# Performance work log

Measured on AMD Instinct MI355X. Metric: run time of the kernel, lower is better.

## Reference

```python
import jax, jax.numpy as jnp
import numpy as np

N_HEADS = 16
D_MODEL = 1024
D_K = D_MODEL // N_HEADS
B, T = 2, 2048


def setup_inputs() -> dict:
    key = jax.random.key(0)
    ks = jax.random.split(key, 12)
    s = 1.0 / np.sqrt(D_MODEL)
    inp = {
        "q": jax.random.normal(ks[0], (B, T, D_MODEL), jnp.float32),
        "k": jax.random.normal(ks[1], (B, T, D_MODEL), jnp.float32),
        "v": jax.random.normal(ks[2], (B, T, D_MODEL), jnp.float32),
        # weights stored as [in, out] (torch Linear weight transposed)
        "Wq": jax.random.normal(ks[3], (D_MODEL, D_MODEL), jnp.float32) * s,
        "bq": jax.random.normal(ks[4], (D_MODEL,), jnp.float32) * s,
        "Wk": jax.random.normal(ks[5], (D_MODEL, D_MODEL), jnp.float32) * s,
        "bk": jax.random.normal(ks[6], (D_MODEL,), jnp.float32) * s,
        "Wv": jax.random.normal(ks[7], (D_MODEL, D_MODEL), jnp.float32) * s,
        "bv": jax.random.normal(ks[8], (D_MODEL,), jnp.float32) * s,
        "Wo": jax.random.normal(ks[9], (D_MODEL, D_MODEL), jnp.float32) * s,
        "bo": jax.random.normal(ks[10], (D_MODEL,), jnp.float32) * s,
        "alpha": jnp.ones((1, N_HEADS, 1, 1), jnp.float32) * 10.0,
    }
    return inp


def reference(q, k, v, Wq, bq, Wk, bk, Wv, bv, Wo, bo, alpha):
    Bsz, Tlen, _ = q.shape

    def proj(x, W, b):
        # [B,T,D] -> [B,H,T,d_k]
        y = x @ W + b
        return y.reshape(Bsz, Tlen, N_HEADS, D_K).transpose(0, 2, 1, 3)

    qh = proj(q, Wq, bq)
    kh = proj(k, Wk, bk)
    vh = proj(v, Wv, bv)

    scores = jnp.einsum("bhqd,bhkd->bhqk", qh, kh)  # [B,H,T,T]
    norm_q = jnp.linalg.norm(qh, axis=-1)  # [B,H,T]
    norm_k = jnp.linalg.norm(kh, axis=-1)  # [B,H,T]
    D_udps = (norm_q[..., :, None] + norm_k[..., None, :]) ** 2  # [B,H,T,T]
    D_safe = jnp.where(D_udps == 0.0, jnp.inf, D_udps)
    scores = alpha * 4.0 * scores / D_safe
    attn = jax.nn.softmax(scores, axis=-1)
    out = jnp.einsum("bhqk,bhkd->bhqd", attn, vh)
    out = out.transpose(0, 2, 1, 3).reshape(Bsz, Tlen, D_MODEL)
    return out @ Wo + bo
```

## Files before the change

kernel.cpp:

```cpp
#include <hip/hip_runtime.h>
#include <hip/hip_bf16.h>

#define N_HEADS 16
#define D_MODEL 1024
#define D_K     64
#define B_SZ    2
#define T_LEN   2048
#define M_ROWS  (B_SZ * T_LEN)

typedef __bf16 bf16;
typedef __bf16 bf16x4 __attribute__((ext_vector_type(4)));
typedef __bf16 bf16x8 __attribute__((ext_vector_type(8)));
typedef float  f32x4  __attribute__((ext_vector_type(4)));
typedef unsigned int u32;

__device__ __forceinline__ void gload16(const bf16* g, bf16* l) {
    __builtin_amdgcn_global_load_lds(
        (const __attribute__((address_space(1))) u32*)g,
        (__attribute__((address_space(3))) u32*)l, 16, 0, 0);
}

__global__ void wt_kernel(const float* __restrict__ W0, const float* __restrict__ W1,
                          const float* __restrict__ W2, const float* __restrict__ W3,
                          bf16* __restrict__ T0, bf16* __restrict__ T1,
                          bf16* __restrict__ T2, bf16* __restrict__ T3) {
    __shared__ float tile[32][33];
    const int z = blockIdx.z;
    const float* W = (z == 0) ? W0 : (z == 1) ? W1 : (z == 2) ? W2 : W3;
    bf16* Wt       = (z == 0) ? T0 : (z == 1) ? T1 : (z == 2) ? T2 : T3;
    const int tx = threadIdx.x, ty = threadIdx.y;
    const int x0 = blockIdx.x * 32, y0 = blockIdx.y * 32;
    for (int yy = ty; yy < 32; yy += 8)
        tile[yy][tx] = W[(size_t)(y0 + yy) * D_MODEL + x0 + tx];
    __syncthreads();
    for (int yy = ty; yy < 32; yy += 8)
        Wt[(size_t)(x0 + yy) * D_MODEL + y0 + tx] = (bf16)tile[tx][yy];
}

__global__ void conv3_kernel(const float* __restrict__ q, const float* __restrict__ k,
                             const float* __restrict__ v,
                             bf16* __restrict__ qb, bf16* __restrict__ kb,
                             bf16* __restrict__ vb) {
    const int z = blockIdx.y;
    const float* X = (z == 0) ? q : (z == 1) ? k : v;
    bf16* Y        = (z == 0) ? qb : (z == 1) ? kb : vb;
    const size_t i = ((size_t)blockIdx.x * 256 + threadIdx.x) * 8;
    const float4 v0 = *(const float4*)&X[i];
    const float4 v1 = *(const float4*)&X[i + 4];
    bf16x8 y;
    y[0]=(bf16)v0.x; y[1]=(bf16)v0.y; y[2]=(bf16)v0.z; y[3]=(bf16)v0.w;
    y[4]=(bf16)v1.x; y[5]=(bf16)v1.y; y[6]=(bf16)v1.z; y[7]=(bf16)v1.w;
    *(bf16x8*)&Y[i] = y;
}

__global__ __launch_bounds__(256, 3) void proj_kernel(
    const bf16* __restrict__ qb, const bf16* __restrict__ kb, const bf16* __restrict__ vb,
    const bf16* __restrict__ WtQ, const bf16* __restrict__ WtK, const bf16* __restrict__ WtV,
    const float* __restrict__ bqp, const float* __restrict__ bkp, const float* __restrict__ bvp,
    bf16* __restrict__ qh, bf16* __restrict__ kh, bf16* __restrict__ vt)
{
    __shared__ bf16 As[2][128 * 32];
    __shared__ bf16 Bs[2][128 * 32];

    const int hw      = blockIdx.x;
    const int logical = (hw & 7) * 96 + (hw >> 3);
    const int z       = logical >> 8;
    const int r       = logical & 255;
    const int m0      = (r >> 3) * 128;
    const int n0      = (r & 7) * 128;

    const bf16*  A    = (z == 0) ? qb  : (z == 1) ? kb  : vb;
    const bf16*  Bt   = (z == 0) ? WtQ : (z == 1) ? WtK : WtV;
    const float* bias = (z == 0) ? bqp : (z == 1) ? bkp : bvp;
    bf16* Out         = (z == 0) ? qh  : (z == 1) ? kh  : vt;

    const int tid = threadIdx.x, lane = tid & 63, w = tid >> 6;
    const int wm = w >> 1, wn = w & 1, g = lane >> 4, c = lane & 15;

    const int srow = w * 32 + (lane >> 2);
    const int scol = (lane & 3) * 8;
    const bf16* Ag = A  + (size_t)(m0 + srow) * D_MODEL + scol;
    const bf16* Bg = Bt + (size_t)(n0 + srow) * D_MODEL + scol;

    f32x4 acc[4][4] = {};

#define PSTAGE(buf, kk)                                                         \
    do {                                                                        \
        gload16(Ag + (kk),                  &As[buf][(w * 32) * 32]);           \
        gload16(Ag + 16 * D_MODEL + (kk),   &As[buf][(w * 32 + 16) * 32]);      \
        gload16(Bg + (kk),                  &Bs[buf][(w * 32) * 32]);           \
        gload16(Bg + 16 * D_MODEL + (kk),   &Bs[buf][(w * 32 + 16) * 32]);      \
    } while (0)

    PSTAGE(0, 0);
    __syncthreads();

    int cur = 0;
    for (int t = 0; t < 32; ++t) {
        if (t < 31) PSTAGE(cur ^ 1, (t + 1) * 32);

        bf16x8 a[4], b[4];
        #pragma unroll
        for (int i = 0; i < 4; i++) a[i] = *(const bf16x8*)&As[cur][(wm*64 + i*16 + c) * 32 + g*8];
        #pragma unroll
        for (int j = 0; j < 4; j++) b[j] = *(const bf16x8*)&Bs[cur][(wn*64 + j*16 + c) * 32 + g*8];

        __builtin_amdgcn_s_setprio(1);
        if (z != 2) {
            #pragma unroll
            for (int i = 0; i < 4; i++)
                #pragma unroll
                for (int j = 0; j < 4; j++)
                    acc[i][j] = __builtin_amdgcn_mfma_f32_16x16x32_bf16(a[i], b[j], acc[i][j], 0, 0, 0);
        } else {
            #pragma unroll
            for (int i = 0; i < 4; i++)
                #pragma unroll
                for (int j = 0; j < 4; j++)
                    acc[i][j] = __builtin_amdgcn_mfma_f32_16x16x32_bf16(b[j], a[i], acc[i][j], 0, 0, 0);
        }
        __builtin_amdgcn_s_setprio(0);
        __syncthreads();
        cur ^= 1;
    }
#undef PSTAGE

    #pragma unroll
    for (int i = 0; i < 4; i++)
        #pragma unroll
        for (int j = 0; j < 4; j++)
            #pragma unroll
            for (int r4 = 0; r4 < 4; r4++) {
                if (z != 2) {
                    const int mrow = m0 + wm*64 + i*16 + g*4 + r4;
                    const int ncol = n0 + wn*64 + j*16 + c;
                    const float y = acc[i][j][r4] + bias[ncol];
                    const int b_ = mrow >> 11, t_ = mrow & (T_LEN - 1);
                    const int h_ = ncol >> 6,  d_ = ncol & (D_K - 1);
                    Out[(((size_t)(b_*N_HEADS + h_))*T_LEN + t_)*D_K + d_] = (bf16)y;
                } else {
                    const int nrow = n0 + wn*64 + j*16 + g*4 + r4;
                    const int mcol = m0 + wm*64 + i*16 + c;
                    const float y = acc[i][j][r4] + bias[nrow];
                    const int b_ = mcol >> 11, t_ = mcol & (T_LEN - 1);
                    const int h_ = nrow >> 6,  d_ = nrow & (D_K - 1);
                    Out[(((size_t)(b_*N_HEADS + h_))*D_K + d_)*T_LEN + t_] = (bf16)y;
                }
            }
}

__global__ void norm_kernel(const bf16* __restrict__ qh, const bf16* __restrict__ kh,
                            float* __restrict__ nq, float* __restrict__ nk, int nrows) {
    const bf16* X = blockIdx.y ? kh : qh;
    float* O      = blockIdx.y ? nk : nq;
    const int row  = blockIdx.x * 4 + (threadIdx.x >> 6);
    const int lane = threadIdx.x & 63;
    if (row >= nrows) return;
    float v = (float)X[(size_t)row * D_K + lane];
    float s = v * v;
    #pragma unroll
    for (int m = 1; m < 64; m <<= 1) s += __shfl_xor(s, m, 64);
    if (lane == 0) O[row] = sqrtf(s);
}

#define KVB 64

__global__ __launch_bounds__(512, 4) void attn_kernel(
    const bf16* __restrict__ qh, const bf16* __restrict__ kh, const bf16* __restrict__ vt,
    const float* __restrict__ nq, const float* __restrict__ nk,
    const float* __restrict__ alpha, bf16* __restrict__ ao)
{
    __shared__ bf16 Ks[2][KVB * D_K];
    __shared__ bf16 Vs[2][KVB * D_K];
    __shared__ bf16 plds[8][16][72];

    const int bid     = blockIdx.x;
    const int logical = (bid & 7) * 64 + (bid >> 3);
    const int bh      = logical >> 4;
    const int q0b     = (logical & 15) * 128;

    const int tid  = threadIdx.x;
    const int w    = tid >> 6;
    const int lane = tid & 63;
    const int g    = lane >> 4, c = lane & 15;
    const int myq  = q0b + w * 16 + c;
    const int sw   = (c & 7) << 4;

    const int srow = tid >> 3;
    const int sgb  = (((tid & 7) ^ (srow & 7)) << 4);

    const bf16* Q  = qh + (size_t)bh * T_LEN * D_K;
    const bf16* K  = kh + (size_t)bh * T_LEN * D_K;
    const bf16* V  = vt + (size_t)bh * D_K * T_LEN;
    const float* NK = nk + (size_t)bh * T_LEN;

    const float al   = alpha[bh & (N_HEADS - 1)];
    const float a4   = al * 4.0f * 1.44269504f;
    const float negM = -(al * 1.44269504f) - 1e-4f;

    const bf16x8 bq0 = *(const bf16x8*)&Q[(size_t)myq * D_K + g*8];
    const bf16x8 bq1 = *(const bf16x8*)&Q[(size_t)myq * D_K + 32 + g*8];
    const float nq_own = nq[(size_t)bh * T_LEN + myq];

    bf16x8 ones;
    #pragma unroll
    for (int e = 0; e < 8; e++) ones[e] = (bf16)1.0f;

    f32x4 o[4] = {};
    f32x4 o4  = {};

    gload16((const bf16*)((const char*)&K[(size_t)srow * D_K] + sgb), &Ks[0][w * 512]);
    gload16((const bf16*)((const char*)&V[(size_t)srow * T_LEN] + sgb), &Vs[0][w * 512]);
    __syncthreads();

    const int NT = T_LEN / KVB;
    int cur = 0;
    for (int t = 0; t < NT; ++t) {
        const int k0 = t * KVB;
        if (t + 1 < NT) {
            const int kn = k0 + KVB;
            gload16((const bf16*)((const char*)&K[(size_t)(kn + srow) * D_K] + sgb), &Ks[cur^1][w * 512]);
            gload16((const bf16*)((const char*)&V[(size_t)srow * T_LEN + kn] + sgb), &Vs[cur^1][w * 512]);
        }

        f32x4 S[4];
        __builtin_amdgcn_s_setprio(1);
        #pragma unroll
        for (int cb = 0; cb < 4; cb++) {
            const char* kbase = (const char*)&Ks[cur][(size_t)(cb*16 + c) * D_K];
            const bf16x8 ka = *(const bf16x8*)(kbase + ((g*16) ^ sw));
            const bf16x8 kb = *(const bf16x8*)(kbase + ((64 + g*16) ^ sw));
            f32x4 s = {};
            s = __builtin_amdgcn_mfma_f32_16x16x32_bf16(ka, bq0, s, 0, 0, 0);
            s = __builtin_amdgcn_mfma_f32_16x16x32_bf16(kb, bq1, s, 0, 0, 0);
            S[cb] = s;
        }
        __builtin_amdgcn_s_setprio(0);

        #pragma unroll
        for (int cb = 0; cb < 4; cb++) {
            const float4 nk4 = *(const float4*)&NK[k0 + cb*16 + g*4];
            const float nkr[4] = {nk4.x, nk4.y, nk4.z, nk4.w};
            bf16x4 pk;
            #pragma unroll
            for (int r = 0; r < 4; r++) {
                const float den = nq_own + nkr[r];
                const float rr  = __builtin_amdgcn_rcpf(den);
                const float x   = __builtin_fmaf(a4 * S[cb][r], rr * rr, negM);
                pk[r] = (bf16)__builtin_amdgcn_exp2f(x);
            }
            *(bf16x4*)&plds[w][c][cb*16 + g*4] = pk;
        }

        __builtin_amdgcn_s_setprio(1);
        #pragma unroll
        for (int ks = 0; ks < 2; ks++) {
            const bf16x8 pb = *(const bf16x8*)&plds[w][c][ks*32 + g*8];
            #pragma unroll
            for (int f = 0; f < 4; f++) {
                const char* vbase = (const char*)&Vs[cur][(size_t)(f*16 + c) * D_K];
                const bf16x8 vb = *(const bf16x8*)(vbase + ((ks*64 + g*16) ^ sw));
                o[f] = __builtin_amdgcn_mfma_f32_16x16x32_bf16(vb, pb, o[f], 0, 0, 0);
            }
            o4 = __builtin_amdgcn_mfma_f32_16x16x32_bf16(ones, pb, o4, 0, 0, 0);
        }
        __builtin_amdgcn_s_setprio(0);

        __syncthreads();
        cur ^= 1;
    }

    const int b_ = bh >> 4, h_ = bh & 15;
    const float inv = 1.0f / o4[0];
    #pragma unroll
    for (int f = 0; f < 4; f++) {
        bf16x4 w4;
        #pragma unroll
        for (int r = 0; r < 4; r++) w4[r] = (bf16)(o[f][r] * inv);
        *(bf16x4*)&ao[((size_t)(b_*T_LEN + myq))*D_MODEL + h_*D_K + f*16 + g*4] = w4;
    }
}

__global__ __launch_bounds__(256, 4) void gemmo_kernel(
    const bf16* __restrict__ A, const bf16* __restrict__ Bt,
    const float* __restrict__ bias, float* __restrict__ Out)
{
    __shared__ bf16 As[2][64 * 32];
    __shared__ bf16 Bs[2][128 * 32];

    const int hw      = blockIdx.x;
    const int logical = (hw & 7) * 64 + (hw >> 3);
    const int m0      = (logical >> 3) * 64;
    const int n0      = (logical & 7) * 128;

    const int tid = threadIdx.x, lane = tid & 63, w = tid >> 6;
    const int wm = w >> 1, wn = w & 1, g = lane >> 4, c = lane & 15;

    const int arow = w * 16 + (lane >> 2);
    const int brow = w * 32 + (lane >> 2);
    const int scol = (lane & 3) * 8;
    const bf16* Ag = A  + (size_t)(m0 + arow) * D_MODEL + scol;
    const bf16* Bg = Bt + (size_t)(n0 + brow) * D_MODEL + scol;

    f32x4 acc[2][4] = {};

#define OSTAGE(buf, kk)                                                         \
    do {                                                                        \
        gload16(Ag + (kk),                &As[buf][(w * 16) * 32]);             \
        gload16(Bg + (kk),                &Bs[buf][(w * 32) * 32]);             \
        gload16(Bg + 16 * D_MODEL + (kk), &Bs[buf][(w * 32 + 16) * 32]);        \
    } while (0)

    OSTAGE(0, 0);
    __syncthreads();

    int cur = 0;
    for (int t = 0; t < 32; ++t) {
        if (t < 31) OSTAGE(cur ^ 1, (t + 1) * 32);

        bf16x8 a[2], b[4];
        #pragma unroll
        for (int i = 0; i < 2; i++) a[i] = *(const bf16x8*)&As[cur][(wm*32 + i*16 + c) * 32 + g*8];
        #pragma unroll
        for (int j = 0; j < 4; j++) b[j] = *(const bf16x8*)&Bs[cur][(wn*64 + j*16 + c) * 32 + g*8];

        __builtin_amdgcn_s_setprio(1);
        #pragma unroll
        for (int i = 0; i < 2; i++)
            #pragma unroll
            for (int j = 0; j < 4; j++)
                acc[i][j] = __builtin_amdgcn_mfma_f32_16x16x32_bf16(a[i], b[j], acc[i][j], 0, 0, 0);
        __builtin_amdgcn_s_setprio(0);
        __syncthreads();
        cur ^= 1;
    }
#undef OSTAGE

    #pragma unroll
    for (int i = 0; i < 2; i++)
        #pragma unroll
        for (int j = 0; j < 4; j++) {
            const int ncol = n0 + wn*64 + j*16 + c;
            const float bb = bias[ncol];
            #pragma unroll
            for (int r = 0; r < 4; r++) {
                const int mrow = m0 + wm*32 + i*16 + g*4 + r;
                Out[(size_t)mrow * D_MODEL + ncol] = acc[i][j][r] + bb;
            }
        }
}

extern "C" void kernel_launch(void* const* d_in, const int* in_sizes, int n_in,
                              void* d_out, int out_size, void* d_ws, size_t ws_size,
                              hipStream_t stream) {
    const float* q     = (const float*)d_in[0];
    const float* k     = (const float*)d_in[1];
    const float* v     = (const float*)d_in[2];
    const float* Wq    = (const float*)d_in[3];
    const float* bq    = (const float*)d_in[4];
    const float* Wk    = (const float*)d_in[5];
    const float* bk    = (const float*)d_in[6];
    const float* Wv    = (const float*)d_in[7];
    const float* bv    = (const float*)d_in[8];
    const float* Wo    = (const float*)d_in[9];
    const float* bo    = (const float*)d_in[10];
    const float* alpha = (const float*)d_in[11];

    char* ws = (char*)d_ws;
    const size_t WBYTES = (size_t)D_MODEL * D_MODEL * sizeof(bf16);
    const size_t HBYTES = (size_t)B_SZ * N_HEADS * T_LEN * D_K * sizeof(bf16);
    const size_t NBYTES = (size_t)B_SZ * N_HEADS * T_LEN * sizeof(float);
    bf16* WtQ = (bf16*)ws;  ws += WBYTES;
    bf16* WtK = (bf16*)ws;  ws += WBYTES;
    bf16* WtV = (bf16*)ws;  ws += WBYTES;
    bf16* WtO = (bf16*)ws;  ws += WBYTES;
    bf16* qh  = (bf16*)ws;  ws += HBYTES;
    bf16* kh  = (bf16*)ws;  ws += HBYTES;
    bf16* vt  = (bf16*)ws;  ws += HBYTES;
    float* nq = (float*)ws; ws += NBYTES;
    float* nk = (float*)ws; ws += NBYTES;
    bf16* ao  = (bf16*)ws;  ws += HBYTES;
    bf16* qb  = (bf16*)ws;  ws += HBYTES;
    bf16* kb  = (bf16*)ws;  ws += HBYTES;
    bf16* vb  = ao;

    wt_kernel<<<dim3(32, 32, 4), dim3(32, 8), 0, stream>>>(
        Wq, Wk, Wv, Wo, WtQ, WtK, WtV, WtO);

    conv3_kernel<<<dim3(M_ROWS * D_MODEL / 8 / 256, 3), 256, 0, stream>>>(
        q, k, v, qb, kb, vb);

    proj_kernel<<<768, 256, 0, stream>>>(
        qb, kb, vb, WtQ, WtK, WtV, bq, bk, bv, qh, kh, vt);

    const int nrows = B_SZ * N_HEADS * T_LEN;
    norm_kernel<<<dim3(nrows / 4, 2), 256, 0, stream>>>(qh, kh, nq, nk, nrows);

    attn_kernel<<<512, 512, 0, stream>>>(qh, kh, vt, nq, nk, alpha, ao);

    gemmo_kernel<<<512, 256, 0, stream>>>(ao, WtO, bo, (float*)d_out);
}
```

Before: 183.6 us.

## Triple-buffer projection and attention LDS stages with explicit vmcnt waits

Both the QKV projection GEMM and the attention kernel move from double to triple buffering, prefetching two stages ahead. The full __syncthreads is replaced by a partial s_waitcnt vmcnt plus a raw s_barrier, so the next stage's loads can stay in flight across the barrier. The attention kernel also hoists the per-tile norm_k loads to the top of the iteration so their latency overlaps the QK MFMAs. This costs 50% more LDS per block, which may reduce occupancy, and the hand-set vmcnt values must match the exact number of outstanding loads.

```diff
diff --git a/kernel.cpp b/kernel.cpp
--- a/kernel.cpp
+++ b/kernel.cpp
@@ -19,6 +19,8 @@
         (const __attribute__((address_space(1))) u32*)g,
         (__attribute__((address_space(3))) u32*)l, 16, 0, 0);
 }
+
+#define WAIT_VM(N) asm volatile("s_waitcnt vmcnt(" #N ")" ::: "memory")
 
 __global__ void wt_kernel(const float* __restrict__ W0, const float* __restrict__ W1,
                           const float* __restrict__ W2, const float* __restrict__ W3,
@@ -59,8 +61,8 @@
     const float* __restrict__ bqp, const float* __restrict__ bkp, const float* __restrict__ bvp,
     bf16* __restrict__ qh, bf16* __restrict__ kh, bf16* __restrict__ vt)
 {
-    __shared__ bf16 As[2][128 * 32];
-    __shared__ bf16 Bs[2][128 * 32];
+    __shared__ bf16 As[3][128 * 32];
+    __shared__ bf16 Bs[3][128 * 32];
 
     const int hw      = blockIdx.x;
     const int logical = (hw & 7) * 96 + (hw >> 3);
@@ -93,11 +95,16 @@
     } while (0)
 
     PSTAGE(0, 0);
-    __syncthreads();
+    PSTAGE(1, 32);
+    WAIT_VM(4);
+    __builtin_amdgcn_s_barrier();
 
     int cur = 0;
     for (int t = 0; t < 32; ++t) {
-        if (t < 31) PSTAGE(cur ^ 1, (t + 1) * 32);
+        if (t + 2 < 32) {
+            int pre = cur + 2; if (pre >= 3) pre -= 3;
+            PSTAGE(pre, (t + 2) * 32);
+        }
 
         bf16x8 a[4], b[4];
         #pragma unroll
@@ -120,8 +127,11 @@
                     acc[i][j] = __builtin_amdgcn_mfma_f32_16x16x32_bf16(b[j], a[i], acc[i][j], 0, 0, 0);
         }
         __builtin_amdgcn_s_setprio(0);
-        __syncthreads();
-        cur ^= 1;
+
+        if (t + 2 < 32) { WAIT_VM(4); }
+        else            { WAIT_VM(0); }
+        __builtin_amdgcn_s_barrier();
+        cur = (cur + 1 == 3) ? 0 : cur + 1;
     }
 #undef PSTAGE
 
@@ -170,8 +180,8 @@
     const float* __restrict__ nq, const float* __restrict__ nk,
     const float* __restrict__ alpha, bf16* __restrict__ ao)
 {
-    __shared__ bf16 Ks[2][KVB * D_K];
-    __shared__ bf16 Vs[2][KVB * D_K];
+    __shared__ bf16 Ks[3][KVB * D_K];
+    __shared__ bf16 Vs[3][KVB * D_K];
     __shared__ bf16 plds[8][16][72];
 
     const int bid     = blockIdx.x;
@@ -209,18 +219,30 @@
     f32x4 o[4] = {};
     f32x4 o4  = {};
 
-    gload16((const bf16*)((const char*)&K[(size_t)srow * D_K] + sgb), &Ks[0][w * 512]);
-    gload16((const bf16*)((const char*)&V[(size_t)srow * T_LEN] + sgb), &Vs[0][w * 512]);
-    __syncthreads();
+#define AKSTAGE(buf, kn)                                                                          \
+    do {                                                                                          \
+        gload16((const bf16*)((const char*)&K[(size_t)((kn) + srow) * D_K] + sgb), &Ks[buf][w * 512]); \
+        gload16((const bf16*)((const char*)&V[(size_t)srow * T_LEN + (kn)] + sgb), &Vs[buf][w * 512]); \
+    } while (0)
+
+    AKSTAGE(0, 0);
+    AKSTAGE(1, KVB);
+    WAIT_VM(2);
+    __builtin_amdgcn_s_barrier();
 
     const int NT = T_LEN / KVB;
     int cur = 0;
     for (int t = 0; t < NT; ++t) {
         const int k0 = t * KVB;
-        if (t + 1 < NT) {
-            const int kn = k0 + KVB;
-            gload16((const bf16*)((const char*)&K[(size_t)(kn + srow) * D_K] + sgb), &Ks[cur^1][w * 512]);
-            gload16((const bf16*)((const char*)&V[(size_t)srow * T_LEN + kn] + sgb), &Vs[cur^1][w * 512]);
+
+        float4 nk4[4];
+        #pragma unroll
+        for (int cb = 0; cb < 4; cb++) nk4[cb] = *(const float4*)&NK[k0 + cb*16 + g*4];
+        __builtin_amdgcn_sched_barrier(0);
+
+        if (t + 2 < NT) {
+            int pre = cur + 2; if (pre >= 3) pre -= 3;
+            AKSTAGE(pre, k0 + 2*KVB);
         }
 
         f32x4 S[4];
@@ -239,8 +261,7 @@
 
         #pragma unroll
         for (int cb = 0; cb < 4; cb++) {
-            const float4 nk4 = *(const float4*)&NK[k0 + cb*16 + g*4];
-            const float nkr[4] = {nk4.x, nk4.y, nk4.z, nk4.w};
+            const float nkr[4] = {nk4[cb].x, nk4[cb].y, nk4[cb].z, nk4[cb].w};
             bf16x4 pk;
             #pragma unroll
             for (int r = 0; r < 4; r++) {
@@ -266,9 +287,12 @@
         }
         __builtin_amdgcn_s_setprio(0);
 
-        __syncthreads();
-        cur ^= 1;
+        if (t + 2 < NT) { WAIT_VM(2); }
+        else            { WAIT_VM(0); }
+        __builtin_amdgcn_s_barrier();
+        cur = (cur + 1 == 3) ? 0 : cur + 1;
     }
+#undef AKSTAGE
 
     const int b_ = bh >> 4, h_ = bh & 15;
     const float inv = 1.0f / o4[0];
```

Result: faster. 170.2 us (-7.3%).
